# Performance work log

Measured on AMD Instinct MI355X. Metric: run time of the kernel, lower is better.

## Reference

```python
import jax, jax.numpy as jnp
import numpy as np

EPS = 1e-5
NUM_GROUPS = 8

def group_norm(x, gamma, beta):
    B, C, D, H, W = x.shape
    g = NUM_GROUPS
    xg = x.reshape(B, g, C // g, D, H, W)
    mu = xg.mean(axis=(2, 3, 4, 5), keepdims=True)
    var = xg.var(axis=(2, 3, 4, 5), keepdims=True)
    xn = ((xg - mu) / jnp.sqrt(var + EPS)).reshape(B, C, D, H, W)
    return xn * gamma[None, :, None, None, None] + beta[None, :, None, None, None]

def setup_inputs() -> dict:
    key = jax.random.key(0)
    ks = jax.random.split(key, 7)
    B, C, D, H, W = 4, 256, 16, 16, 16
    x = jax.random.normal(ks[0], (B, C, D, H, W), dtype=jnp.float32)
    gn_gamma = jnp.ones((C,), dtype=jnp.float32)
    gn_beta = jnp.zeros((C,), dtype=jnp.float32)
    # 1x1x1 conv weights stored as [out, in] matrices
    s = 1.0 / np.sqrt(C)
    qkv_w = jax.random.uniform(ks[1], (3 * C, C), minval=-s, maxval=s, dtype=jnp.float32)
    qkv_b = jax.random.uniform(ks[2], (3 * C,), minval=-s, maxval=s, dtype=jnp.float32)
    proj_w = jax.random.uniform(ks[3], (C, C), minval=-s, maxval=s, dtype=jnp.float32)
    proj_b = jax.random.uniform(ks[4], (C,), minval=-s, maxval=s, dtype=jnp.float32)
    return {"x": x, "gn_gamma": gn_gamma, "gn_beta": gn_beta,
            "qkv_w": qkv_w, "qkv_b": qkv_b, "proj_w": proj_w, "proj_b": proj_b}

def reference(x, gn_gamma, gn_beta, qkv_w, qkv_b, proj_w, proj_b):
    B, C, D, H, W = x.shape
    N = D * H * W
    h = group_norm(x, gn_gamma, gn_beta)
    hf = h.reshape(B, C, N)  # (B, C, N)
    # 1x1x1 conv == channel matmul
    qkv = jnp.einsum('oc,bcn->bon', qkv_w, hf) + qkv_b[None, :, None]  # (B, 3C, N)
    q, k, v = jnp.split(qkv, 3, axis=1)  # each (B, C, N)
    q = q.transpose(0, 2, 1)  # (B, N, C)
    k = k.transpose(0, 2, 1)
    v = v.transpose(0, 2, 1)
    scale = C ** (-0.5)
    attn = jnp.einsum('bnc,bmc->bnm', q, k) * scale  # (B, N, N)
    attn = jax.nn.softmax(attn, axis=-1)
    o = jnp.einsum('bnm,bmc->bnc', attn, v)  # (B, N, C)
    o = o.transpose(0, 2, 1)  # (B, C, N)
    o = jnp.einsum('oc,bcn->bon', proj_w, o) + proj_b[None, :, None]
    return x + o.reshape(B, C, D, H, W)
```

## Files before the change

### kernel.cpp

```cpp
#include <hip/hip_runtime.h>
#include <hip/hip_bf16.h>

typedef unsigned short u16;
typedef unsigned int u32;
typedef __attribute__((ext_vector_type(8))) short short8;
typedef __attribute__((ext_vector_type(4))) short short4v;
typedef __attribute__((ext_vector_type(4))) float f32x4;

static __device__ __forceinline__ u16 f2bf(float f) {
    union { float f; unsigned u; } a; a.f = f;
    unsigned u = a.u;
    u += 0x7FFFu + ((u >> 16) & 1u);
    return (u16)(u >> 16);
}
static __device__ __forceinline__ float bf2f(u16 h) {
    union { u32 u; float f; } a; a.u = ((u32)h) << 16; return a.f;
}
static __device__ __forceinline__ u32 cvtpk(float lo, float hi) {
    u32 r; asm("v_cvt_pk_bf16_f32 %0, %1, %2" : "=v"(r) : "v"(lo), "v"(hi)); return r;
}
static __device__ __forceinline__ void gload16(const u16* g, u16* l) {
    __builtin_amdgcn_global_load_lds((const __attribute__((address_space(1))) u32*)(const void*)g,
                                     (__attribute__((address_space(3))) u32*)(void*)l, 16, 0, 0);
}

__global__ __launch_bounds__(256) void k_pre(const float* __restrict__ x, float* __restrict__ stats,
                                             const float* __restrict__ qw, const float* __restrict__ pw,
                                             u16* __restrict__ q2, u16* __restrict__ p2) {
    const int t = threadIdx.x;
    if (blockIdx.x >= 32) {
        const int i = ((int)blockIdx.x - 32) * 1024 + t * 4;
        const float* src; u16* dst;
        if (i < 196608) { src = qw + i; dst = q2 + i; }
        else            { src = pw + (i - 196608); dst = p2 + (i - 196608); }
        float4 v = *reinterpret_cast<const float4*>(src);
        u16 o[4] = { f2bf(v.x), f2bf(v.y), f2bf(v.z), f2bf(v.w) };
        *reinterpret_cast<uint2*>(dst) = *reinterpret_cast<uint2*>(o);
        return;
    }
    const int bg = blockIdx.x;
    const float* p = x + (size_t)bg * (32 * 4096);
    float s = 0.f, ss = 0.f;
    for (int i = t * 4; i < 32 * 4096; i += 256 * 4) {
        float4 v = *reinterpret_cast<const float4*>(p + i);
        s  += v.x + v.y + v.z + v.w;
        ss += v.x * v.x + v.y * v.y + v.z * v.z + v.w * v.w;
    }
    for (int off = 1; off < 64; off <<= 1) { s += __shfl_xor(s, off); ss += __shfl_xor(ss, off); }
    __shared__ float ls[4], lss[4];
    if ((t & 63) == 0) { ls[t >> 6] = s; lss[t >> 6] = ss; }
    __syncthreads();
    if (t == 0) {
        float S  = ls[0] + ls[1] + ls[2] + ls[3];
        float SS = lss[0] + lss[1] + lss[2] + lss[3];
        const float inv = 1.f / (32.f * 4096.f);
        float mu  = S * inv;
        float var = SS * inv - mu * mu;
        stats[bg * 2]     = mu;
        stats[bg * 2 + 1] = rsqrtf(var + 1e-5f);
    }
}

__global__ __launch_bounds__(256) void k_norm(const float* __restrict__ x, const float* __restrict__ gamma,
                                              const float* __restrict__ beta, const float* __restrict__ stats,
                                              u16* __restrict__ H) {
    __shared__ u16 T[64][72];
    const int b = blockIdx.z, c0 = blockIdx.y * 64, n0 = blockIdx.x * 64;
    const int t = threadIdx.x;
    const int cl = t >> 2, nb = (t & 3) * 16;
    const int c = c0 + cl;
    const float mu = stats[(b * 8 + (c >> 5)) * 2];
    const float rstd = stats[(b * 8 + (c >> 5)) * 2 + 1];
    const float ga = gamma[c] * rstd, be = beta[c] - mu * ga;
    const float* xp = &x[((size_t)b * 256 + c) * 4096 + n0 + nb];
#pragma unroll
    for (int j = 0; j < 16; j += 4) {
        float4 v = *reinterpret_cast<const float4*>(xp + j);
        T[cl][nb + j + 0] = f2bf(v.x * ga + be);
        T[cl][nb + j + 1] = f2bf(v.y * ga + be);
        T[cl][nb + j + 2] = f2bf(v.z * ga + be);
        T[cl][nb + j + 3] = f2bf(v.w * ga + be);
    }
    __syncthreads();
    const int nl = t >> 2, cb = (t & 3) * 16;
    short8 s0, s1;
#pragma unroll
    for (int j = 0; j < 8; ++j) { s0[j] = (short)T[cb + j][nl]; s1[j] = (short)T[cb + 8 + j][nl]; }
    u16* dst = &H[((size_t)b * 4096 + n0 + nl) * 256 + c0 + cb];
    *reinterpret_cast<short8*>(dst)     = s0;
    *reinterpret_cast<short8*>(dst + 8) = s1;
}

__global__ __launch_bounds__(256) void k_qkv(const u16* __restrict__ H, const u16* __restrict__ W2,
                                             const float* __restrict__ qkv_b,
                                             u16* __restrict__ Q, u16* __restrict__ K, u16* __restrict__ V) {
    __shared__ u16 T[9216];
    const int b = blockIdx.z, o0 = blockIdx.x * 64, nb0 = blockIdx.y * 128;
    const int t = threadIdx.x, w = t >> 6, l = t & 63, lr = l & 15, lg = l >> 4;
    const size_t bN = (size_t)b * 4096;
    f32x4 acc[2][4];
#pragma unroll
    for (int m = 0; m < 2; ++m)
#pragma unroll
        for (int nf = 0; nf < 4; ++nf) acc[m][nf] = f32x4{0.f, 0.f, 0.f, 0.f};
    const u16* A0 = &H[(bN + nb0 + w * 32 + lr) * 256];
    const u16* A1 = A0 + 16 * 256;
#pragma unroll
    for (int cc = 0; cc < 8; ++cc) {
        short8 af0 = *reinterpret_cast<const short8*>(A0 + cc * 32 + lg * 8);
        short8 af1 = *reinterpret_cast<const short8*>(A1 + cc * 32 + lg * 8);
#pragma unroll
        for (int nf = 0; nf < 4; ++nf) {
            short8 bf = *reinterpret_cast<const short8*>(&W2[(size_t)(o0 + nf * 16 + lr) * 256 + cc * 32 + lg * 8]);
            acc[0][nf] = __builtin_amdgcn_mfma_f32_16x16x32_bf16(af0, bf, acc[0][nf], 0, 0, 0);
            acc[1][nf] = __builtin_amdgcn_mfma_f32_16x16x32_bf16(af1, bf, acc[1][nf], 0, 0, 0);
        }
    }
    const int og = o0 >> 8;
    const float scal = (og == 0) ? 0.0625f * 1.44269504f : 1.0f;
    float bias[4];
#pragma unroll
    for (int nf = 0; nf < 4; ++nf) bias[nf] = qkv_b[o0 + nf * 16 + lr];
    if (og < 2) {
#pragma unroll
        for (int m = 0; m < 2; ++m)
#pragma unroll
            for (int nf = 0; nf < 4; ++nf)
#pragma unroll
                for (int i = 0; i < 4; ++i)
                    T[(w * 32 + m * 16 + lg * 4 + i) * 72 + nf * 16 + lr] = f2bf((acc[m][nf][i] + bias[nf]) * scal);
        __syncthreads();
        const int rl = t >> 1, half = (t & 1) * 32;
        u16* dst = (og == 0 ? Q : K) + (bN + nb0 + rl) * 256 + (o0 & 255) + half;
#pragma unroll
        for (int j = 0; j < 4; ++j)
            *reinterpret_cast<short8*>(dst + j * 8) = *reinterpret_cast<short8*>(&T[rl * 72 + half + j * 8]);
    } else {
#pragma unroll
        for (int m = 0; m < 2; ++m)
#pragma unroll
            for (int nf = 0; nf < 4; ++nf)
#pragma unroll
                for (int i = 0; i < 4; ++i)
                    T[(nf * 16 + lr) * 144 + w * 32 + m * 16 + lg * 4 + i] = f2bf(acc[m][nf][i] + bias[nf]);
        __syncthreads();
        const int ol = t >> 2, nbl = (t & 3) * 32;
        const int s_ = (ol >> 1) & 7;
        u16* dst = V + ((size_t)b * 256 + (o0 - 512) + ol) * 4096 + nb0 + nbl;
#pragma unroll
        for (int j = 0; j < 4; ++j) {
            short8 vv = *reinterpret_cast<short8*>(&T[ol * 144 + nbl + j * 8]);
            short8 ov;
            if (s_ & 1) ov = short8{vv[4], vv[5], vv[6], vv[7], vv[0], vv[1], vv[2], vv[3]};
            else        ov = vv;
            *reinterpret_cast<short8*>(dst + (((2 * j) ^ (s_ & 6)) * 4)) = ov;
        }
    }
}

__global__ __launch_bounds__(512, 1) void k_flash(const u16* __restrict__ Qw, const u16* __restrict__ Kw,
                                                  const u16* __restrict__ Vw, u16* __restrict__ Opart,
                                                  float* __restrict__ ml) {
    __shared__ u16 Ks[2][16384];
    __shared__ u16 Vs[2][16384];
    const int b = blockIdx.z, sp = blockIdx.y;
    const int tid = threadIdx.x;
    const int w = tid >> 6, l = tid & 63;
    const int lr = l & 15, lg = l >> 4;
    const int qbase = blockIdx.x * 256 + w * 32;
    const int kb0 = sp * 1024;
    const size_t bN = (size_t)b * 4096;

    const u16* srcK = Kw + (bN + kb0 + (tid >> 5)) * 256 + (((tid & 31) * 8) ^ (((tid >> 5) & 7) * 8));
    const u16* srcV = Vw + ((size_t)b * 256 + (tid >> 3)) * 4096 + kb0 + (tid & 7) * 8;

#define STAGE(d, toff) { \
        const u16* sk_ = srcK + (size_t)(toff) * 16384; \
        const u16* sv_ = srcV + (toff) * 64; \
        gload16(sk_,               Ks[d] + tid * 8); \
        gload16(sk_ + 16 * 256,    Ks[d] + 4096 + tid * 8); \
        gload16(sk_ + 32 * 256,    Ks[d] + 8192 + tid * 8); \
        gload16(sk_ + 48 * 256,    Ks[d] + 12288 + tid * 8); \
        gload16(sv_,               Vs[d] + tid * 8); \
        gload16(sv_ + 64 * 4096,   Vs[d] + 4096 + tid * 8); \
        gload16(sv_ + 128 * 4096,  Vs[d] + 8192 + tid * 8); \
        gload16(sv_ + 192 * 4096,  Vs[d] + 12288 + tid * 8); }

    const int c6 = (lr >> 2) & 1;
    int kofs[2];
#pragma unroll
    for (int n = 0; n < 2; ++n) kofs[n] = (n * 16 + lr) * 256 + ((lg * 8) ^ ((lr & 3) * 8));
    const int vslotA = ((lg ^ (lr >> 1)) * 4);
    const int vslotB = vslotA ^ 16;

    short8 qf[2][8];
#pragma unroll
    for (int m = 0; m < 2; ++m)
#pragma unroll
        for (int cc = 0; cc < 8; ++cc)
            qf[m][cc] = *reinterpret_cast<const short8*>(&Qw[(bN + qbase + m * 16 + lr) * 256 + cc * 32 + lg * 8]);

    f32x4 Oa[2][16];
    float mr[2], lsum[2];
#pragma unroll
    for (int m = 0; m < 2; ++m) {
#pragma unroll
        for (int cs = 0; cs < 16; ++cs) Oa[m][cs] = f32x4{0.f, 0.f, 0.f, 0.f};
        mr[m] = -1e30f; lsum[m] = 0.f;
    }

    STAGE(0, 0);
    for (int kt = 0; kt < 16; ++kt) {
        const int d = kt & 1;
        asm volatile("s_waitcnt vmcnt(0)" ::: "memory");
        __builtin_amdgcn_sched_barrier(0);
        __builtin_amdgcn_s_barrier();
        if (kt < 15) STAGE(d ^ 1, kt + 1);

#pragma unroll
        for (int st = 0; st < 2; ++st) {
            const int kO = st * 8192;
            const int vO = st * 32;
            f32x4 sc[2][2];
#pragma unroll
            for (int m = 0; m < 2; ++m)
#pragma unroll
                for (int n = 0; n < 2; ++n) sc[m][n] = f32x4{0.f, 0.f, 0.f, 0.f};
            __builtin_amdgcn_s_setprio(1);
#pragma unroll
            for (int cc = 0; cc < 8; ++cc) {
                const int cb = ((cc ^ c6) << 5);
                short8 kf0 = *reinterpret_cast<const short8*>(&Ks[d][kO + kofs[0] + cb]);
                short8 kf1 = *reinterpret_cast<const short8*>(&Ks[d][kO + kofs[1] + cb]);
                sc[0][0] = __builtin_amdgcn_mfma_f32_16x16x32_bf16(kf0, qf[0][cc], sc[0][0], 0, 0, 0);
                sc[0][1] = __builtin_amdgcn_mfma_f32_16x16x32_bf16(kf1, qf[0][cc], sc[0][1], 0, 0, 0);
                sc[1][0] = __builtin_amdgcn_mfma_f32_16x16x32_bf16(kf0, qf[1][cc], sc[1][0], 0, 0, 0);
                sc[1][1] = __builtin_amdgcn_mfma_f32_16x16x32_bf16(kf1, qf[1][cc], sc[1][1], 0, 0, 0);
            }
            __builtin_amdgcn_s_setprio(0);

            float tmax[2];
            bool need = false;
#pragma unroll
            for (int m = 0; m < 2; ++m) {
                float tm = fmaxf(fmaxf(fmaxf(sc[m][0][0], sc[m][0][1]), fmaxf(sc[m][0][2], sc[m][0][3])),
                                 fmaxf(fmaxf(sc[m][1][0], sc[m][1][1]), fmaxf(sc[m][1][2], sc[m][1][3])));
                tm = fmaxf(tm, __shfl_xor(tm, 16));
                tm = fmaxf(tm, __shfl_xor(tm, 32));
                tmax[m] = tm;
                need = need || (tm > mr[m] + 8.f);
            }
            if (__any(need)) {
                float av[2][4];
#pragma unroll
                for (int m = 0; m < 2; ++m) {
                    float mn = fmaxf(mr[m], tmax[m]);
                    float al = exp2f(mr[m] - mn);
                    mr[m] = mn;
                    lsum[m] *= al;
#pragma unroll
                    for (int i = 0; i < 4; ++i) av[m][i] = __shfl(al, lg * 4 + i);
                }
#pragma unroll
                for (int m = 0; m < 2; ++m)
#pragma unroll
                    for (int cs = 0; cs < 16; ++cs)
#pragma unroll
                        for (int i = 0; i < 4; ++i) Oa[m][cs][i] *= av[m][i];
            }
            union { u32 uw[4]; short8 v; } pf[2];
#pragma unroll
            for (int m = 0; m < 2; ++m) {
                float p[8];
                float la = 0.f;
#pragma unroll
                for (int n = 0; n < 2; ++n)
#pragma unroll
                    for (int i = 0; i < 4; ++i) {
                        float pv = exp2f(sc[m][n][i] - mr[m]);
                        la += pv;
                        p[n * 4 + i] = pv;
                    }
                lsum[m] += la;
#pragma unroll
                for (int j = 0; j < 4; ++j) pf[m].uw[j] = cvtpk(p[2 * j], p[2 * j + 1]);
            }
            __builtin_amdgcn_s_setprio(1);
#pragma unroll
            for (int cs = 0; cs < 16; ++cs) {
                const int base = (cs * 16 + lr) * 64 + vO;
                short4v lo = *reinterpret_cast<const short4v*>(&Vs[d][base + vslotA]);
                short4v hi = *reinterpret_cast<const short4v*>(&Vs[d][base + vslotB]);
                short8 vf = __builtin_shufflevector(lo, hi, 0, 1, 2, 3, 4, 5, 6, 7);
                Oa[0][cs] = __builtin_amdgcn_mfma_f32_16x16x32_bf16(pf[0].v, vf, Oa[0][cs], 0, 0, 0);
                Oa[1][cs] = __builtin_amdgcn_mfma_f32_16x16x32_bf16(pf[1].v, vf, Oa[1][cs], 0, 0, 0);
            }
            __builtin_amdgcn_s_setprio(0);
        }
    }
#undef STAGE

    float lt[2];
#pragma unroll
    for (int m = 0; m < 2; ++m) {
        float ts = lsum[m];
        ts += __shfl_xor(ts, 16);
        ts += __shfl_xor(ts, 32);
        lt[m] = ts;
    }
    const size_t obase = ((size_t)(b * 4 + sp) * 4096 + qbase);
#pragma unroll
    for (int m = 0; m < 2; ++m)
#pragma unroll
        for (int cs = 0; cs < 16; ++cs)
#pragma unroll
            for (int i = 0; i < 4; ++i)
                Opart[(obase + m * 16 + lg * 4 + i) * 256 + cs * 16 + lr] = f2bf(Oa[m][cs][i]);
    if (lg == 0) {
#pragma unroll
        for (int m = 0; m < 2; ++m) {
            size_t r = obase + m * 16 + lr;
            ml[r * 2]     = mr[m];
            ml[r * 2 + 1] = lt[m];
        }
    }
}

__global__ __launch_bounds__(256) void k_comb(const u16* __restrict__ Opart, const float* __restrict__ ml,
                                              u16* __restrict__ Obf) {
    const int row = blockIdx.x * 8 + (threadIdx.x >> 5);
    const int b = row >> 12;
    const int c0 = (threadIdx.x & 31) * 8;
    const size_t rbase = (size_t)b * 4 * 4096 + (row & 4095);
    float ms[4], lsv[4];
#pragma unroll
    for (int s = 0; s < 4; ++s) {
        ms[s]  = ml[(rbase + (size_t)s * 4096) * 2];
        lsv[s] = ml[(rbase + (size_t)s * 4096) * 2 + 1];
    }
    float M = fmaxf(fmaxf(ms[0], ms[1]), fmaxf(ms[2], ms[3]));
    float W[4], L = 0.f;
#pragma unroll
    for (int s = 0; s < 4; ++s) { W[s] = exp2f(ms[s] - M); L += W[s] * lsv[s]; }
    const float inv = 1.f / L;
    float o[8] = {};
#pragma unroll
    for (int s = 0; s < 4; ++s) {
        short8 v = *reinterpret_cast<const short8*>(&Opart[(rbase + (size_t)s * 4096) * 256 + c0]);
#pragma unroll
        for (int j = 0; j < 8; ++j) o[j] += W[s] * bf2f((u16)v[j]);
    }
    short8 r;
#pragma unroll
    for (int j = 0; j < 8; ++j) r[j] = (short)f2bf(o[j] * inv);
    *reinterpret_cast<short8*>(&Obf[(size_t)row * 256 + c0]) = r;
}

__global__ __launch_bounds__(256) void k_proj(const u16* __restrict__ O, const u16* __restrict__ Wp,
                                              const float* __restrict__ proj_b, const float* __restrict__ x,
                                              float* __restrict__ out) {
    __shared__ float T[64][132];
    const int b = blockIdx.z, c0 = blockIdx.x * 64, nb0 = blockIdx.y * 128;
    const int t = threadIdx.x, w = t >> 6, l = t & 63, lr = l & 15, lg = l >> 4;
    const size_t bN = (size_t)b * 4096;
    f32x4 acc[2][4];
#pragma unroll
    for (int m = 0; m < 2; ++m)
#pragma unroll
        for (int nf = 0; nf < 4; ++nf) acc[m][nf] = f32x4{0.f, 0.f, 0.f, 0.f};
    const u16* A0 = &O[(bN + nb0 + w * 32 + lr) * 256];
    const u16* A1 = A0 + 16 * 256;
#pragma unroll
    for (int cc = 0; cc < 8; ++cc) {
        short8 af0 = *reinterpret_cast<const short8*>(A0 + cc * 32 + lg * 8);
        short8 af1 = *reinterpret_cast<const short8*>(A1 + cc * 32 + lg * 8);
#pragma unroll
        for (int nf = 0; nf < 4; ++nf) {
            short8 bf = *reinterpret_cast<const short8*>(&Wp[(size_t)(c0 + nf * 16 + lr) * 256 + cc * 32 + lg * 8]);
            acc[0][nf] = __builtin_amdgcn_mfma_f32_16x16x32_bf16(af0, bf, acc[0][nf], 0, 0, 0);
            acc[1][nf] = __builtin_amdgcn_mfma_f32_16x16x32_bf16(af1, bf, acc[1][nf], 0, 0, 0);
        }
    }
#pragma unroll
    for (int m = 0; m < 2; ++m)
#pragma unroll
        for (int nf = 0; nf < 4; ++nf)
#pragma unroll
            for (int i = 0; i < 4; ++i)
                T[nf * 16 + lr][w * 32 + m * 16 + lg * 4 + i] = acc[m][nf][i];
    __syncthreads();
    const int cl = t >> 2, nbl = (t & 3) * 32;
    const float pb = proj_b[c0 + cl];
    const size_t base = ((size_t)b * 256 + c0 + cl) * 4096 + nb0 + nbl;
#pragma unroll
    for (int j = 0; j < 32; j += 4) {
        float4 xv = *reinterpret_cast<const float4*>(&x[base + j]);
        float4 r;
        r.x = xv.x + T[cl][nbl + j + 0] + pb;
        r.y = xv.y + T[cl][nbl + j + 1] + pb;
        r.z = xv.z + T[cl][nbl + j + 2] + pb;
        r.w = xv.w + T[cl][nbl + j + 3] + pb;
        *reinterpret_cast<float4*>(&out[base + j]) = r;
    }
}

extern "C" void kernel_launch(void* const* d_in, const int* in_sizes, int n_in,
                              void* d_out, int out_size, void* d_ws, size_t ws_size,
                              hipStream_t stream) {
    const float* x      = (const float*)d_in[0];
    const float* gngam  = (const float*)d_in[1];
    const float* gnbeta = (const float*)d_in[2];
    const float* qkv_w  = (const float*)d_in[3];
    const float* qkv_b  = (const float*)d_in[4];
    const float* proj_w = (const float*)d_in[5];
    const float* proj_b = (const float*)d_in[6];
    float* out = (float*)d_out;

    char* wsb = (char*)d_ws;
    float* stats = (float*)wsb;
    u16* Hbf   = (u16*)(wsb + 1024);
    u16* Qws   = Hbf + 4194304;
    u16* Kws   = Qws + 4194304;
    u16* Vws   = Kws + 4194304;
    u16* W2q   = Vws + 4194304;
    u16* W2p   = W2q + 196608;
    u16* Opart = W2p + 65536;
    float* ml  = (float*)(Opart + 16777216);
    u16* Obf   = (u16*)(ml + 131072);

    k_pre<<<288, 256, 0, stream>>>(x, stats, qkv_w, proj_w, W2q, W2p);
    k_norm<<<dim3(64, 4, 4), 256, 0, stream>>>(x, gngam, gnbeta, stats, Hbf);
    k_qkv<<<dim3(12, 32, 4), 256, 0, stream>>>(Hbf, W2q, qkv_b, Qws, Kws, Vws);
    k_flash<<<dim3(16, 4, 4), 512, 0, stream>>>(Qws, Kws, Vws, Opart, ml);
    k_comb<<<2048, 256, 0, stream>>>(Opart, ml, Obf);
    k_proj<<<dim3(4, 32, 4), 256, 0, stream>>>(Obf, W2p, proj_b, x, out);
}
```

Measured before the change: 198.5 us.

## Fuse groupnorm into QKV GEMM and split-combine into projection GEMM

GroupNorm normalization is folded into the QKV kernel, which stages a normalized 64-row tile in LDS and loops over all 12 output tiles. The split-K combine is folded into the projection kernel, which merges the four partial outputs into LDS before the GEMM. The flash grid is reordered so that splits of the same query block are launched adjacently. This removes the H and Obf intermediate buffers and two launches, at the cost of fewer blocks and more serial work per block.

New measurement: 219.2 us. 10.4% more time.

```diff
diff --git a/kernel.cpp b/kernel.cpp
--- a/kernel.cpp
+++ b/kernel.cpp
@@ -61,99 +61,89 @@
     }
 }
 
-__global__ __launch_bounds__(256) void k_norm(const float* __restrict__ x, const float* __restrict__ gamma,
+__global__ __launch_bounds__(256) void k_qkv2(const float* __restrict__ x, const float* __restrict__ gamma,
                                               const float* __restrict__ beta, const float* __restrict__ stats,
-                                              u16* __restrict__ H) {
-    __shared__ u16 T[64][72];
-    const int b = blockIdx.z, c0 = blockIdx.y * 64, n0 = blockIdx.x * 64;
-    const int t = threadIdx.x;
-    const int cl = t >> 2, nb = (t & 3) * 16;
-    const int c = c0 + cl;
-    const float mu = stats[(b * 8 + (c >> 5)) * 2];
-    const float rstd = stats[(b * 8 + (c >> 5)) * 2 + 1];
-    const float ga = gamma[c] * rstd, be = beta[c] - mu * ga;
-    const float* xp = &x[((size_t)b * 256 + c) * 4096 + n0 + nb];
-#pragma unroll
-    for (int j = 0; j < 16; j += 4) {
-        float4 v = *reinterpret_cast<const float4*>(xp + j);
-        T[cl][nb + j + 0] = f2bf(v.x * ga + be);
-        T[cl][nb + j + 1] = f2bf(v.y * ga + be);
-        T[cl][nb + j + 2] = f2bf(v.z * ga + be);
-        T[cl][nb + j + 3] = f2bf(v.w * ga + be);
-    }
-    __syncthreads();
-    const int nl = t >> 2, cb = (t & 3) * 16;
-    short8 s0, s1;
-#pragma unroll
-    for (int j = 0; j < 8; ++j) { s0[j] = (short)T[cb + j][nl]; s1[j] = (short)T[cb + 8 + j][nl]; }
-    u16* dst = &H[((size_t)b * 4096 + n0 + nl) * 256 + c0 + cb];
-    *reinterpret_cast<short8*>(dst)     = s0;
-    *reinterpret_cast<short8*>(dst + 8) = s1;
-}
-
-__global__ __launch_bounds__(256) void k_qkv(const u16* __restrict__ H, const u16* __restrict__ W2,
-                                             const float* __restrict__ qkv_b,
-                                             u16* __restrict__ Q, u16* __restrict__ K, u16* __restrict__ V) {
-    __shared__ u16 T[9216];
-    const int b = blockIdx.z, o0 = blockIdx.x * 64, nb0 = blockIdx.y * 128;
+                                              const u16* __restrict__ W2, const float* __restrict__ qkv_b,
+                                              u16* __restrict__ Q, u16* __restrict__ K, u16* __restrict__ V) {
+    __shared__ u16 A[64 * 272];
+    __shared__ u16 T[64 * 72];
+    const int b = blockIdx.y, n0 = blockIdx.x * 64;
     const int t = threadIdx.x, w = t >> 6, l = t & 63, lr = l & 15, lg = l >> 4;
     const size_t bN = (size_t)b * 4096;
-    f32x4 acc[2][4];
-#pragma unroll
-    for (int m = 0; m < 2; ++m)
-#pragma unroll
-        for (int nf = 0; nf < 4; ++nf) acc[m][nf] = f32x4{0.f, 0.f, 0.f, 0.f};
-    const u16* A0 = &H[(bN + nb0 + w * 32 + lr) * 256];
-    const u16* A1 = A0 + 16 * 256;
-#pragma unroll
-    for (int cc = 0; cc < 8; ++cc) {
-        short8 af0 = *reinterpret_cast<const short8*>(A0 + cc * 32 + lg * 8);
-        short8 af1 = *reinterpret_cast<const short8*>(A1 + cc * 32 + lg * 8);
-#pragma unroll
-        for (int nf = 0; nf < 4; ++nf) {
-            short8 bf = *reinterpret_cast<const short8*>(&W2[(size_t)(o0 + nf * 16 + lr) * 256 + cc * 32 + lg * 8]);
-            acc[0][nf] = __builtin_amdgcn_mfma_f32_16x16x32_bf16(af0, bf, acc[0][nf], 0, 0, 0);
-            acc[1][nf] = __builtin_amdgcn_mfma_f32_16x16x32_bf16(af1, bf, acc[1][nf], 0, 0, 0);
-        }
-    }
-    const int og = o0 >> 8;
-    const float scal = (og == 0) ? 0.0625f * 1.44269504f : 1.0f;
-    float bias[4];
-#pragma unroll
-    for (int nf = 0; nf < 4; ++nf) bias[nf] = qkv_b[o0 + nf * 16 + lr];
-    if (og < 2) {
-#pragma unroll
-        for (int m = 0; m < 2; ++m)
+
+    {
+        const int cq = t >> 2;
+        const int na = (t & 3) * 4;
+#pragma unroll
+        for (int p = 0; p < 4; ++p) {
+            const int c = p * 64 + cq;
+            const float mu = stats[(b * 8 + (c >> 5)) * 2];
+            const float rstd = stats[(b * 8 + (c >> 5)) * 2 + 1];
+            const float ga = gamma[c] * rstd, be = beta[c] - mu * ga;
+            const float* xp = &x[((size_t)b * 256 + c) * 4096 + n0];
+#pragma unroll
+            for (int j = 0; j < 4; ++j) {
+                float4 v = *reinterpret_cast<const float4*>(xp + na + j * 16);
+                const int n = na + j * 16;
+                A[(n + 0) * 272 + c] = f2bf(v.x * ga + be);
+                A[(n + 1) * 272 + c] = f2bf(v.y * ga + be);
+                A[(n + 2) * 272 + c] = f2bf(v.z * ga + be);
+                A[(n + 3) * 272 + c] = f2bf(v.w * ga + be);
+            }
+        }
+    }
+    __syncthreads();
+    short8 af[8];
+#pragma unroll
+    for (int cc = 0; cc < 8; ++cc)
+        af[cc] = *reinterpret_cast<const short8*>(&A[(w * 16 + lr) * 272 + cc * 32 + lg * 8]);
+
+    for (int ot = 0; ot < 12; ++ot) {
+        const int o0 = ot * 64;
+        f32x4 acc[4];
+#pragma unroll
+        for (int nf = 0; nf < 4; ++nf) acc[nf] = f32x4{0.f, 0.f, 0.f, 0.f};
+#pragma unroll
+        for (int cc = 0; cc < 8; ++cc) {
+#pragma unroll
+            for (int nf = 0; nf < 4; ++nf) {
+                short8 bf = *reinterpret_cast<const short8*>(&W2[(size_t)(o0 + nf * 16 + lr) * 256 + cc * 32 + lg * 8]);
+                acc[nf] = __builtin_amdgcn_mfma_f32_16x16x32_bf16(af[cc], bf, acc[nf], 0, 0, 0);
+            }
+        }
+        float bias[4];
+#pragma unroll
+        for (int nf = 0; nf < 4; ++nf) bias[nf] = qkv_b[o0 + nf * 16 + lr];
+        if (ot < 8) {
+            const float scal = (ot < 4) ? 0.0625f * 1.44269504f : 1.0f;
 #pragma unroll
             for (int nf = 0; nf < 4; ++nf)
 #pragma unroll
                 for (int i = 0; i < 4; ++i)
-                    T[(w * 32 + m * 16 + lg * 4 + i) * 72 + nf * 16 + lr] = f2bf((acc[m][nf][i] + bias[nf]) * scal);
-        __syncthreads();
-        const int rl = t >> 1, half = (t & 1) * 32;
-        u16* dst = (og == 0 ? Q : K) + (bN + nb0 + rl) * 256 + (o0 & 255) + half;
-#pragma unroll
-        for (int j = 0; j < 4; ++j)
-            *reinterpret_cast<short8*>(dst + j * 8) = *reinterpret_cast<short8*>(&T[rl * 72 + half + j * 8]);
-    } else {
-#pragma unroll
-        for (int m = 0; m < 2; ++m)
+                    T[(w * 16 + lg * 4 + i) * 72 + nf * 16 + lr] = f2bf((acc[nf][i] + bias[nf]) * scal);
+            __syncthreads();
+            const int rl = t >> 2, cb = (t & 3) * 16;
+            u16* dst = (ot < 4 ? Q : K) + (bN + n0 + rl) * 256 + (o0 & 255) + cb;
+            *reinterpret_cast<short8*>(dst)     = *reinterpret_cast<short8*>(&T[rl * 72 + cb]);
+            *reinterpret_cast<short8*>(dst + 8) = *reinterpret_cast<short8*>(&T[rl * 72 + cb + 8]);
+            __syncthreads();
+        } else {
 #pragma unroll
             for (int nf = 0; nf < 4; ++nf)
 #pragma unroll
                 for (int i = 0; i < 4; ++i)
-                    T[(nf * 16 + lr) * 144 + w * 32 + m * 16 + lg * 4 + i] = f2bf(acc[m][nf][i] + bias[nf]);
-        __syncthreads();
-        const int ol = t >> 2, nbl = (t & 3) * 32;
-        const int s_ = (ol >> 1) & 7;
-        u16* dst = V + ((size_t)b * 256 + (o0 - 512) + ol) * 4096 + nb0 + nbl;
-#pragma unroll
-        for (int j = 0; j < 4; ++j) {
-            short8 vv = *reinterpret_cast<short8*>(&T[ol * 144 + nbl + j * 8]);
-            short8 ov;
-            if (s_ & 1) ov = short8{vv[4], vv[5], vv[6], vv[7], vv[0], vv[1], vv[2], vv[3]};
-            else        ov = vv;
-            *reinterpret_cast<short8*>(dst + (((2 * j) ^ (s_ & 6)) * 4)) = ov;
+                    T[(nf * 16 + lr) * 72 + w * 16 + lg * 4 + i] = f2bf(acc[nf][i] + bias[nf]);
+            __syncthreads();
+            const int ol = t >> 2, nbl = (t & 3) * 16;
+            const int s_ = (ol >> 1) & 7;
+            u16* dst = V + ((size_t)b * 256 + (o0 - 512) + ol) * 4096 + n0 + (nbl & 32);
+#pragma unroll
+            for (int j = 0; j < 4; ++j) {
+                const int g = (((nbl & 31) >> 2) + j) & 7;
+                *reinterpret_cast<uint2*>(dst + ((g ^ s_) * 4)) =
+                    *reinterpret_cast<uint2*>(&T[ol * 72 + nbl + j * 4]);
+            }
+            __syncthreads();
         }
     }
 }
@@ -163,11 +153,11 @@
                                                   float* __restrict__ ml) {
     __shared__ u16 Ks[2][16384];
     __shared__ u16 Vs[2][16384];
-    const int b = blockIdx.z, sp = blockIdx.y;
+    const int sp = blockIdx.x, b = blockIdx.y;
     const int tid = threadIdx.x;
     const int w = tid >> 6, l = tid & 63;
     const int lr = l & 15, lg = l >> 4;
-    const int qbase = blockIdx.x * 256 + w * 32;
+    const int qbase = blockIdx.z * 256 + w * 32;
     const int kb0 = sp * 1024;
     const size_t bN = (size_t)b * 4096;
 
@@ -326,81 +316,97 @@
     }
 }
 
-__global__ __launch_bounds__(256) void k_comb(const u16* __restrict__ Opart, const float* __restrict__ ml,
-                                              u16* __restrict__ Obf) {
-    const int row = blockIdx.x * 8 + (threadIdx.x >> 5);
-    const int b = row >> 12;
-    const int c0 = (threadIdx.x & 31) * 8;
-    const size_t rbase = (size_t)b * 4 * 4096 + (row & 4095);
-    float ms[4], lsv[4];
-#pragma unroll
-    for (int s = 0; s < 4; ++s) {
-        ms[s]  = ml[(rbase + (size_t)s * 4096) * 2];
-        lsv[s] = ml[(rbase + (size_t)s * 4096) * 2 + 1];
-    }
-    float M = fmaxf(fmaxf(ms[0], ms[1]), fmaxf(ms[2], ms[3]));
-    float W[4], L = 0.f;
-#pragma unroll
-    for (int s = 0; s < 4; ++s) { W[s] = exp2f(ms[s] - M); L += W[s] * lsv[s]; }
-    const float inv = 1.f / L;
-    float o[8] = {};
-#pragma unroll
-    for (int s = 0; s < 4; ++s) {
-        short8 v = *reinterpret_cast<const short8*>(&Opart[(rbase + (size_t)s * 4096) * 256 + c0]);
-#pragma unroll
-        for (int j = 0; j < 8; ++j) o[j] += W[s] * bf2f((u16)v[j]);
-    }
-    short8 r;
-#pragma unroll
-    for (int j = 0; j < 8; ++j) r[j] = (short)f2bf(o[j] * inv);
-    *reinterpret_cast<short8*>(&Obf[(size_t)row * 256 + c0]) = r;
-}
-
-__global__ __launch_bounds__(256) void k_proj(const u16* __restrict__ O, const u16* __restrict__ Wp,
-                                              const float* __restrict__ proj_b, const float* __restrict__ x,
-                                              float* __restrict__ out) {
-    __shared__ float T[64][132];
-    const int b = blockIdx.z, c0 = blockIdx.x * 64, nb0 = blockIdx.y * 128;
+__global__ __launch_bounds__(256) void k_proj2(const u16* __restrict__ Opart, const float* __restrict__ ml,
+                                               const u16* __restrict__ Wp, const float* __restrict__ proj_b,
+                                               const float* __restrict__ x, float* __restrict__ out) {
+    __shared__ u16 A[64 * 272];
+    __shared__ float Wl[64][4];
+    __shared__ float T3[64][68];
+    const int b = blockIdx.y, n0 = blockIdx.x * 64;
     const int t = threadIdx.x, w = t >> 6, l = t & 63, lr = l & 15, lg = l >> 4;
-    const size_t bN = (size_t)b * 4096;
-    f32x4 acc[2][4];
-#pragma unroll
-    for (int m = 0; m < 2; ++m)
-#pragma unroll
-        for (int nf = 0; nf < 4; ++nf) acc[m][nf] = f32x4{0.f, 0.f, 0.f, 0.f};
-    const u16* A0 = &O[(bN + nb0 + w * 32 + lr) * 256];
-    const u16* A1 = A0 + 16 * 256;
-#pragma unroll
-    for (int cc = 0; cc < 8; ++cc) {
-        short8 af0 = *reinterpret_cast<const short8*>(A0 + cc * 32 + lg * 8);
-        short8 af1 = *reinterpret_cast<const short8*>(A1 + cc * 32 + lg * 8);
-#pragma unroll
-        for (int nf = 0; nf < 4; ++nf) {
-            short8 bf = *reinterpret_cast<const short8*>(&Wp[(size_t)(c0 + nf * 16 + lr) * 256 + cc * 32 + lg * 8]);
-            acc[0][nf] = __builtin_amdgcn_mfma_f32_16x16x32_bf16(af0, bf, acc[0][nf], 0, 0, 0);
-            acc[1][nf] = __builtin_amdgcn_mfma_f32_16x16x32_bf16(af1, bf, acc[1][nf], 0, 0, 0);
-        }
-    }
-#pragma unroll
-    for (int m = 0; m < 2; ++m)
+
+    if (t < 64) {
+        const size_t r0 = (size_t)(b * 4) * 4096 + n0 + t;
+        float m[4], lv[4];
+#pragma unroll
+        for (int s = 0; s < 4; ++s) {
+            m[s]  = ml[(r0 + (size_t)s * 4096) * 2];
+            lv[s] = ml[(r0 + (size_t)s * 4096) * 2 + 1];
+        }
+        float M = fmaxf(fmaxf(m[0], m[1]), fmaxf(m[2], m[3]));
+        float W[4], L = 0.f;
+#pragma unroll
+        for (int s = 0; s < 4; ++s) { W[s] = exp2f(m[s] - M); L += W[s] * lv[s]; }
+        const float inv = 1.f / L;
+#pragma unroll
+        for (int s = 0; s < 4; ++s) Wl[t][s] = W[s] * inv;
+    }
+    __syncthreads();
+
+    {
+        const int cseg = (t & 31) * 8;
+        const int nr = t >> 5;
+#pragma unroll
+        for (int p = 0; p < 8; ++p) {
+            const int n = p * 8 + nr;
+            const float w0 = Wl[n][0], w1 = Wl[n][1], w2 = Wl[n][2], w3 = Wl[n][3];
+            const u16* bp = &Opart[((size_t)(b * 4) * 4096 + n0 + n) * 256 + cseg];
+            short8 v0 = *reinterpret_cast<const short8*>(bp);
+            short8 v1 = *reinterpret_cast<const short8*>(bp + (size_t)4096 * 256);
+            short8 v2 = *reinterpret_cast<const short8*>(bp + (size_t)2 * 4096 * 256);
+            short8 v3 = *reinterpret_cast<const short8*>(bp + (size_t)3 * 4096 * 256);
+            union { u32 uw[4]; short8 v; } pk;
+#pragma unroll
+            for (int jj = 0; jj < 4; ++jj) {
+                float oa = w0 * bf2f((u16)v0[2 * jj])     + w1 * bf2f((u16)v1[2 * jj])
+                         + w2 * bf2f((u16)v2[2 * jj])     + w3 * bf2f((u16)v3[2 * jj]);
+                float ob = w0 * bf2f((u16)v0[2 * jj + 1]) + w1 * bf2f((u16)v1[2 * jj + 1])
+                         + w2 * bf2f((u16)v2[2 * jj + 1]) + w3 * bf2f((u16)v3[2 * jj + 1]);
+                pk.uw[jj] = cvtpk(oa, ob);
+            }
+            *reinterpret_cast<short8*>(&A[n * 272 + cseg]) = pk.v;
+        }
+    }
+    __syncthreads();
+
+    short8 af[8];
+#pragma unroll
+    for (int cc = 0; cc < 8; ++cc)
+        af[cc] = *reinterpret_cast<const short8*>(&A[(w * 16 + lr) * 272 + cc * 32 + lg * 8]);
+
+    for (int ct = 0; ct < 4; ++ct) {
+        const int c0 = ct * 64;
+        f32x4 acc[4];
+#pragma unroll
+        for (int nf = 0; nf < 4; ++nf) acc[nf] = f32x4{0.f, 0.f, 0.f, 0.f};
+#pragma unroll
+        for (int cc = 0; cc < 8; ++cc) {
+#pragma unroll
+            for (int nf = 0; nf < 4; ++nf) {
+                short8 bf = *reinterpret_cast<const short8*>(&Wp[(size_t)(c0 + nf * 16 + lr) * 256 + cc * 32 + lg * 8]);
+                acc[nf] = __builtin_amdgcn_mfma_f32_16x16x32_bf16(af[cc], bf, acc[nf], 0, 0, 0);
+            }
+        }
 #pragma unroll
         for (int nf = 0; nf < 4; ++nf)
 #pragma unroll
             for (int i = 0; i < 4; ++i)
-                T[nf * 16 + lr][w * 32 + m * 16 + lg * 4 + i] = acc[m][nf][i];
-    __syncthreads();
-    const int cl = t >> 2, nbl = (t & 3) * 32;
-    const float pb = proj_b[c0 + cl];
-    const size_t base = ((size_t)b * 256 + c0 + cl) * 4096 + nb0 + nbl;
-#pragma unroll
-    for (int j = 0; j < 32; j += 4) {
-        float4 xv = *reinterpret_cast<const float4*>(&x[base + j]);
-        float4 r;
-        r.x = xv.x + T[cl][nbl + j + 0] + pb;
-        r.y = xv.y + T[cl][nbl + j + 1] + pb;
-        r.z = xv.z + T[cl][nbl + j + 2] + pb;
-        r.w = xv.w + T[cl][nbl + j + 3] + pb;
-        *reinterpret_cast<float4*>(&out[base + j]) = r;
+                T3[nf * 16 + lr][w * 16 + lg * 4 + i] = acc[nf][i];
+        __syncthreads();
+        const int cl = t >> 2, nbl = (t & 3) * 16;
+        const float pb = proj_b[c0 + cl];
+        const size_t base = ((size_t)b * 256 + c0 + cl) * 4096 + n0 + nbl;
+#pragma unroll
+        for (int j = 0; j < 16; j += 4) {
+            float4 xv = *reinterpret_cast<const float4*>(&x[base + j]);
+            float4 r;
+            r.x = xv.x + T3[cl][nbl + j + 0] + pb;
+            r.y = xv.y + T3[cl][nbl + j + 1] + pb;
+            r.z = xv.z + T3[cl][nbl + j + 2] + pb;
+            r.w = xv.w + T3[cl][nbl + j + 3] + pb;
+            *reinterpret_cast<float4*>(&out[base + j]) = r;
+        }
+        __syncthreads();
     }
 }
 
@@ -418,20 +424,16 @@
 
     char* wsb = (char*)d_ws;
     float* stats = (float*)wsb;
-    u16* Hbf   = (u16*)(wsb + 1024);
-    u16* Qws   = Hbf + 4194304;
+    u16* Qws   = (u16*)(wsb + 1024);
     u16* Kws   = Qws + 4194304;
     u16* Vws   = Kws + 4194304;
     u16* W2q   = Vws + 4194304;
     u16* W2p   = W2q + 196608;
     u16* Opart = W2p + 65536;
     float* ml  = (float*)(Opart + 16777216);
-    u16* Obf   = (u16*)(ml + 131072);
 
     k_pre<<<288, 256, 0, stream>>>(x, stats, qkv_w, proj_w, W2q, W2p);
-    k_norm<<<dim3(64, 4, 4), 256, 0, stream>>>(x, gngam, gnbeta, stats, Hbf);
-    k_qkv<<<dim3(12, 32, 4), 256, 0, stream>>>(Hbf, W2q, qkv_b, Qws, Kws, Vws);
-    k_flash<<<dim3(16, 4, 4), 512, 0, stream>>>(Qws, Kws, Vws, Opart, ml);
-    k_comb<<<2048, 256, 0, stream>>>(Opart, ml, Obf);
-    k_proj<<<dim3(4, 32, 4), 256, 0, stream>>>(Obf, W2p, proj_b, x, out);
-}
+    k_qkv2<<<dim3(64, 4), 256, 0, stream>>>(x, gngam, gnbeta, stats, W2q, qkv_b, Qws, Kws, Vws);
+    k_flash<<<dim3(4, 4, 16), 512, 0, stream>>>(Qws, Kws, Vws, Opart, ml);
+    k_proj2<<<dim3(64, 4), 256, 0, stream>>>(Opart, ml, W2p, proj_b, x, out);
+}
```
